# Performance work log

Hardware: AMD Instinct MI355X
Metric: run time of the kernel (lower is better)

Reference implementation:

```python
import jax, jax.numpy as jnp
import numpy as np

TEMPERATURE = 0.5
EPS = 1e-20


def setup_inputs() -> dict:
    key = jax.random.key(0)
    ks = jax.random.split(key, 7)
    N, T, S = 16, 64, 1024
    SRC, TGT, D = 512, 512, 64
    return {
        "input": jax.random.normal(ks[0], (N, T, TGT), jnp.float32),
        "memory_bank": jax.random.normal(ks[1], (N, S, SRC), jnp.float32),
        "W_q": jax.random.normal(ks[2], (TGT, D), jnp.float32) / np.sqrt(TGT),
        "W_ctx": jax.random.normal(ks[3], (SRC, D), jnp.float32) / np.sqrt(SRC),
        "v": jax.random.normal(ks[4], (D,), jnp.float32) / np.sqrt(D),
        "W_out": jax.random.normal(ks[5], (SRC + TGT, TGT), jnp.float32) / np.sqrt(SRC + TGT),
        "b_out": jax.random.normal(ks[6], (TGT,), jnp.float32) * 0.01,
    }


def reference(input, memory_bank, W_q, W_ctx, v, W_out, b_out):
    # MLP attention score: v^T tanh(W_q q + W_ctx h)
    wq = jnp.einsum("ntd,de->nte", input, W_q)            # [N,T,D]
    uh = jnp.einsum("nsd,de->nse", memory_bank, W_ctx)    # [N,S,D]
    wquh = jnp.tanh(wq[:, :, None, :] + uh[:, None, :, :])  # [N,T,S,D]
    scores = jnp.einsum("ntsd,d->nts", wquh, v)           # [N,T,S]

    log_alpha = jax.nn.log_softmax(scores, axis=-1)
    alpha = jnp.exp(log_alpha)                            # c_align_vectors

    # deterministic context + output
    context_c = jnp.einsum("nts,nsd->ntd", alpha, memory_bank)
    h_c = jnp.tanh(jnp.concatenate([input, context_c], axis=-1) @ W_out + b_out)

    # gumbel-softmax sample (K = n_samples = 1, forced by view_as in original)
    u = jax.random.uniform(jax.random.key(42), log_alpha.shape, jnp.float32)
    g = -jnp.log(-jnp.log(u + EPS) + EPS)                 # gumbel noise
    y_align = jax.nn.softmax((log_alpha + g) / TEMPERATURE, axis=-1)  # [N,T,S]

    context_y = jnp.einsum("nts,nsd->ntd", y_align, memory_bank)
    h_y = jnp.tanh(jnp.concatenate([input, context_y], axis=-1) @ W_out + b_out)

    return jnp.stack([h_c, h_y], axis=0)  # [2,N,T,tgt_dim]
```

## Files before the change

kernel.cpp:

```cpp
#include <hip/hip_runtime.h>
#include <hip/hip_bf16.h>
#include <stdint.h>

#define DEV __device__ __forceinline__

typedef __attribute__((ext_vector_type(8))) short short8;
typedef __attribute__((ext_vector_type(4))) float f32x4;

#define TWO_LOG2E 2.8853900817779268f

DEV unsigned short f2bf(float f) {
  uint32_t u = __float_as_uint(f);
  u += 0x7FFFu + ((u >> 16) & 1u);
  return (unsigned short)(u >> 16);
}

DEV uint2 pk4(float4 f) {
  union { __hip_bfloat162 h; unsigned u; } a, b;
  a.h = __float22bfloat162_rn(make_float2(f.x, f.y));
  b.h = __float22bfloat162_rn(make_float2(f.z, f.w));
  return make_uint2(a.u, b.u);
}

DEV short8 mk8(uint2 lo, uint2 hi) {
  union { short8 s; uint4 u; } t;
  t.u = make_uint4(lo.x, lo.y, hi.x, hi.y);
  return t.s;
}

DEV uint32_t rotl32(uint32_t x, int r) { return (x << r) | (x >> (32 - r)); }

DEV void threefry_0_42(uint32_t x0, uint32_t x1, uint32_t& o0, uint32_t& o1) {
  const uint32_t ks0 = 0u, ks1 = 42u, ks2 = 0x1BD11BDAu ^ 42u;
  x0 += ks0; x1 += ks1;
#define TFR(r) { x0 += x1; x1 = rotl32(x1, (r)); x1 ^= x0; }
  TFR(13) TFR(15) TFR(26) TFR(6)  x0 += ks1; x1 += ks2 + 1u;
  TFR(17) TFR(29) TFR(16) TFR(24) x0 += ks2; x1 += ks0 + 2u;
  TFR(13) TFR(15) TFR(26) TFR(6)  x0 += ks0; x1 += ks1 + 3u;
  TFR(17) TFR(29) TFR(16) TFR(24) x0 += ks1; x1 += ks2 + 4u;
  TFR(13) TFR(15) TFR(26) TFR(6)  x0 += ks2; x1 += ks0 + 5u;
#undef TFR
  o0 = x0; o1 = x1;
}

DEV float wredmax(float v) {
#pragma unroll
  for (int off = 32; off > 0; off >>= 1) v = fmaxf(v, __shfl_xor(v, off));
  return v;
}
DEV float wredsum(float v) {
#pragma unroll
  for (int off = 32; off > 0; off >>= 1) v += __shfl_xor(v, off);
  return v;
}

__global__ __launch_bounds__(256) void transpose_all(const float* __restrict__ Wctx,
                                                     const float* __restrict__ Wq,
                                                     const float* __restrict__ Wout,
                                                     unsigned short* __restrict__ WctxT,
                                                     unsigned short* __restrict__ WqT,
                                                     unsigned short* __restrict__ WoutT) {
  __shared__ float tile[64][65];
  const int b = blockIdx.x;
  const float* src; unsigned short* dst; int R, C, br, bc;
  if (b < 8)       { src = Wctx; dst = WctxT; R = 512;  C = 64;  br = b * 64;        bc = 0; }
  else if (b < 16) { src = Wq;   dst = WqT;   R = 512;  C = 64;  br = (b - 8) * 64;  bc = 0; }
  else { int i = b - 16; src = Wout; dst = WoutT; R = 1024; C = 512; br = (i & 15) * 64; bc = (i >> 4) * 64; }
  const int tid = threadIdx.x;
  const int lr = tid >> 4, lc4 = (tid & 15) * 4;
#pragma unroll
  for (int i = 0; i < 4; ++i) {
    float4 v = *(const float4*)(src + (long)(br + lr + i * 16) * C + bc + lc4);
    tile[lr + i * 16][lc4 + 0] = v.x;
    tile[lr + i * 16][lc4 + 1] = v.y;
    tile[lr + i * 16][lc4 + 2] = v.z;
    tile[lr + i * 16][lc4 + 3] = v.w;
  }
  __syncthreads();
#pragma unroll
  for (int i = 0; i < 4; ++i) {
    int crow = lr + i * 16;
    ushort4 o;
    o.x = f2bf(tile[lc4 + 0][crow]);
    o.y = f2bf(tile[lc4 + 1][crow]);
    o.z = f2bf(tile[lc4 + 2][crow]);
    o.w = f2bf(tile[lc4 + 3][crow]);
    *(ushort4*)(dst + (long)(bc + crow) * R + br + lc4) = o;
  }
}

__global__ __launch_bounds__(256) void gemm_uhwq(const float* __restrict__ mb,
                                                 const float* __restrict__ input,
                                                 const unsigned short* __restrict__ WctxT,
                                                 const unsigned short* __restrict__ WqT,
                                                 float* __restrict__ uhT,
                                                 float* __restrict__ wqo) {
  __shared__ unsigned short As[64][32];
  __shared__ unsigned short Bs[64][32];
  const int tid = threadIdx.x;
  const int bx = blockIdx.x;
  const float* A;  const unsigned short* BT;  int mbase;
  if (bx < 256) { A = mb;    BT = WctxT; mbase = bx * 64; }
  else          { A = input; BT = WqT;   mbase = (bx - 256) * 64; }
  const int srow = tid >> 2, kc = tid & 3;
  const int scol = ((kc ^ (srow & 3)) * 8);
  const int wave = tid >> 6, lane = tid & 63;
  const int wm = (wave >> 1) * 32, wn = (wave & 1) * 32;
  const int q = lane >> 4, r = lane & 15;
  const int c0 = ((q ^ (r & 3)) * 8);
  const float* ap = A + (long)(mbase + srow) * 512 + kc * 8;
  const unsigned short* bp = BT + (long)srow * 512 + kc * 8;
  f32x4 acc[2][2];
#pragma unroll
  for (int i = 0; i < 2; ++i)
#pragma unroll
    for (int j = 0; j < 2; ++j) acc[i][j] = (f32x4){0.f, 0.f, 0.f, 0.f};

  float4 fa0 = *(const float4*)(ap);
  float4 fa1 = *(const float4*)(ap + 4);
  uint4 fb = *(const uint4*)(bp);
  for (int k0 = 0; k0 < 512; k0 += 32) {
    uint2 p0 = pk4(fa0), p1 = pk4(fa1);
    *(uint4*)&As[srow][scol] = make_uint4(p0.x, p0.y, p1.x, p1.y);
    *(uint4*)&Bs[srow][scol] = fb;
    __syncthreads();
    if (k0 + 32 < 512) {
      fa0 = *(const float4*)(ap + k0 + 32);
      fa1 = *(const float4*)(ap + k0 + 36);
      fb = *(const uint4*)(bp + k0 + 32);
    }
    short8 a0 = *(const short8*)&As[wm + r][c0];
    short8 a1 = *(const short8*)&As[wm + 16 + r][c0];
    short8 b0 = *(const short8*)&Bs[wn + r][c0];
    short8 b1 = *(const short8*)&Bs[wn + 16 + r][c0];
    acc[0][0] = __builtin_amdgcn_mfma_f32_16x16x32_bf16(a0, b0, acc[0][0], 0, 0, 0);
    acc[0][1] = __builtin_amdgcn_mfma_f32_16x16x32_bf16(a0, b1, acc[0][1], 0, 0, 0);
    acc[1][0] = __builtin_amdgcn_mfma_f32_16x16x32_bf16(a1, b0, acc[1][0], 0, 0, 0);
    acc[1][1] = __builtin_amdgcn_mfma_f32_16x16x32_bf16(a1, b1, acc[1][1], 0, 0, 0);
    __syncthreads();
  }
#pragma unroll
  for (int i2 = 0; i2 < 2; ++i2)
#pragma unroll
    for (int j2 = 0; j2 < 2; ++j2) {
      int gcol = wn + j2 * 16 + r;
      int m = mbase + wm + i2 * 16 + q * 4;
      if (bx < 256) {
        int n = m >> 10, s0 = m & 1023;
        float4 o;
        o.x = acc[i2][j2][0] * TWO_LOG2E;
        o.y = acc[i2][j2][1] * TWO_LOG2E;
        o.z = acc[i2][j2][2] * TWO_LOG2E;
        o.w = acc[i2][j2][3] * TWO_LOG2E;
        *(float4*)(uhT + (long)n * 65536 + (long)gcol * 1024 + s0) = o;
      } else {
#pragma unroll
        for (int reg = 0; reg < 4; ++reg)
          wqo[(long)(m + reg) * 64 + gcol] = acc[i2][j2][reg] * TWO_LOG2E;
      }
    }
}

__global__ __launch_bounds__(256) void gemm_ctx_mfma(const float* __restrict__ alpha,
                                                     const float* __restrict__ yal,
                                                     const float* __restrict__ mb,
                                                     float* __restrict__ ctx) {
  __shared__ unsigned short As[64][32];
  const int tid = threadIdx.x;
  const int vt = blockIdx.x >> 4, n = blockIdx.x & 15;
  const int dbase = blockIdx.y * 32;
  const int srow = tid >> 2, kc = tid & 3;
  const int scol = ((kc ^ (srow & 3)) * 8);
  const int wave = tid >> 6, lane = tid & 63;
  const int wm = (wave >> 1) * 32, wn = (wave & 1) * 16;
  const int q = lane >> 4, r = lane & 15;
  const int c0 = ((q ^ (r & 3)) * 8);
  const float* Abase = (vt == 0 ? alpha : yal) + (long)n * 65536;
  const float* ap = Abase + (long)srow * 1024 + kc * 8;
  const float* bcol = mb + (long)n * 524288 + dbase + wn + r;
  f32x4 acc[2];
  acc[0] = (f32x4){0.f, 0.f, 0.f, 0.f};
  acc[1] = (f32x4){0.f, 0.f, 0.f, 0.f};

  float4 fa0 = *(const float4*)(ap);
  float4 fa1 = *(const float4*)(ap + 4);
  float bv[8];
#pragma unroll
  for (int j = 0; j < 8; ++j) bv[j] = bcol[(long)(q * 8 + j) * 512];

  for (int k0 = 0; k0 < 1024; k0 += 32) {
    uint2 p0 = pk4(fa0), p1 = pk4(fa1);
    *(uint4*)&As[srow][scol] = make_uint4(p0.x, p0.y, p1.x, p1.y);
    __syncthreads();
    float4 blo = make_float4(bv[0], bv[1], bv[2], bv[3]);
    float4 bhi = make_float4(bv[4], bv[5], bv[6], bv[7]);
    short8 b0 = mk8(pk4(blo), pk4(bhi));
    if (k0 + 32 < 1024) {
      fa0 = *(const float4*)(ap + k0 + 32);
      fa1 = *(const float4*)(ap + k0 + 36);
#pragma unroll
      for (int j = 0; j < 8; ++j) bv[j] = bcol[(long)(k0 + 32 + q * 8 + j) * 512];
    }
    short8 a0 = *(const short8*)&As[wm + r][c0];
    short8 a1 = *(const short8*)&As[wm + 16 + r][c0];
    acc[0] = __builtin_amdgcn_mfma_f32_16x16x32_bf16(a0, b0, acc[0], 0, 0, 0);
    acc[1] = __builtin_amdgcn_mfma_f32_16x16x32_bf16(a1, b0, acc[1], 0, 0, 0);
    __syncthreads();
  }
#pragma unroll
  for (int i2 = 0; i2 < 2; ++i2) {
    int gcol = dbase + wn + r;
#pragma unroll
    for (int reg = 0; reg < 4; ++reg) {
      long grow = (long)vt * 1024 + n * 64 + wm + i2 * 16 + q * 4 + reg;
      ctx[grow * 512 + gcol] = acc[i2][reg];
    }
  }
}

__global__ __launch_bounds__(256) void gemm_out_mfma(const float* __restrict__ input,
                                                     const float* __restrict__ ctx,
                                                     const unsigned short* __restrict__ WoutT,
                                                     const float* __restrict__ bout,
                                                     float* __restrict__ out) {
  __shared__ unsigned short As[64][32];
  __shared__ unsigned short Bs[32][32];
  const int tid = threadIdx.x;
  const int mbase = blockIdx.x * 64, nbase = blockIdx.y * 32;
  const int srow = tid >> 2, kc = tid & 3;
  const int scol = ((kc ^ (srow & 3)) * 8);
  const int wave = tid >> 6, lane = tid & 63;
  const int wm = (wave >> 1) * 32, wn = (wave & 1) * 16;
  const int q = lane >> 4, r = lane & 15;
  const int c0 = ((q ^ (r & 3)) * 8);
  const int vv = mbase >> 10, nt = (mbase + srow) & 1023;
  const float* ap_lo = input + (long)nt * 512 + kc * 8;
  const float* ap_hi = ctx + (long)(vv * 1024 + nt) * 512 + kc * 8 - 512;
  const int brow = (tid & 127) >> 2;
  const unsigned short* bp = WoutT + (long)(nbase + brow) * 1024 + kc * 8;
  f32x4 acc[2];
  acc[0] = (f32x4){0.f, 0.f, 0.f, 0.f};
  acc[1] = (f32x4){0.f, 0.f, 0.f, 0.f};

  float4 fa0 = *(const float4*)(ap_lo);
  float4 fa1 = *(const float4*)(ap_lo + 4);
  uint4 fb;
  if (tid < 128) fb = *(const uint4*)(bp);
  for (int k0 = 0; k0 < 1024; k0 += 32) {
    uint2 p0 = pk4(fa0), p1 = pk4(fa1);
    *(uint4*)&As[srow][scol] = make_uint4(p0.x, p0.y, p1.x, p1.y);
    if (tid < 128) *(uint4*)&Bs[brow][(kc ^ (brow & 3)) * 8] = fb;
    __syncthreads();
    int kn = k0 + 32;
    if (kn < 1024) {
      const float* apn = (kn < 512) ? ap_lo : ap_hi;
      fa0 = *(const float4*)(apn + kn);
      fa1 = *(const float4*)(apn + kn + 4);
      if (tid < 128) fb = *(const uint4*)(bp + kn);
    }
    short8 a0 = *(const short8*)&As[wm + r][c0];
    short8 a1 = *(const short8*)&As[wm + 16 + r][c0];
    short8 b0 = *(const short8*)&Bs[wn + r][c0];
    acc[0] = __builtin_amdgcn_mfma_f32_16x16x32_bf16(a0, b0, acc[0], 0, 0, 0);
    acc[1] = __builtin_amdgcn_mfma_f32_16x16x32_bf16(a1, b0, acc[1], 0, 0, 0);
    __syncthreads();
  }
#pragma unroll
  for (int i2 = 0; i2 < 2; ++i2) {
    int gcol = nbase + wn + r;
    float bb = bout[gcol];
#pragma unroll
    for (int reg = 0; reg < 4; ++reg) {
      int grow = mbase + wm + i2 * 16 + q * 4 + reg;
      float z = acc[i2][reg] + bb;
      float rc = __builtin_amdgcn_rcpf(1.f + __builtin_amdgcn_exp2f(z * TWO_LOG2E));
      out[(long)grow * 512 + gcol] = fmaf(-2.f, rc, 1.f);
    }
  }
}

__global__ __launch_bounds__(256) void scores_kernel(const float* __restrict__ uhT,
                                                     const float* __restrict__ wq2,
                                                     const float* __restrict__ v,
                                                     float* __restrict__ alpha_g,
                                                     float* __restrict__ y_g) {
  const int tid = threadIdx.x;
  const int nt = blockIdx.x;
  const int n = nt >> 6;
  __shared__ float wvs[64];
  __shared__ float vvs[64];
  __shared__ float red[4];
  if (tid < 64) {
    wvs[tid] = wq2[nt * 64 + tid];
    vvs[tid] = v[tid];
  }
  __syncthreads();

  float sumv = 0.f;
#pragma unroll
  for (int d = 0; d < 64; d += 4) {
    float4 vv = *(const float4*)&vvs[d];
    sumv += vv.x + vv.y + vv.z + vv.w;
  }

  const float* un = uhT + (long)n * 65536 + tid * 4;
  float4 racc = make_float4(0.f, 0.f, 0.f, 0.f);
  for (int db = 0; db < 64; db += 8) {
    float4 ub[8];
#pragma unroll
    for (int j = 0; j < 8; ++j) ub[j] = *(const float4*)(un + (long)(db + j) * 1024);
#pragma unroll
    for (int j = 0; j < 8; ++j) {
      float w = wvs[db + j], vvj = vvs[db + j];
      racc.x = fmaf(vvj, __builtin_amdgcn_rcpf(1.f + __builtin_amdgcn_exp2f(ub[j].x + w)), racc.x);
      racc.y = fmaf(vvj, __builtin_amdgcn_rcpf(1.f + __builtin_amdgcn_exp2f(ub[j].y + w)), racc.y);
      racc.z = fmaf(vvj, __builtin_amdgcn_rcpf(1.f + __builtin_amdgcn_exp2f(ub[j].z + w)), racc.z);
      racc.w = fmaf(vvj, __builtin_amdgcn_rcpf(1.f + __builtin_amdgcn_exp2f(ub[j].w + w)), racc.w);
    }
  }
  float lsc[4];
  lsc[0] = fmaf(-2.f, racc.x, sumv);
  lsc[1] = fmaf(-2.f, racc.y, sumv);
  lsc[2] = fmaf(-2.f, racc.z, sumv);
  lsc[3] = fmaf(-2.f, racc.w, sumv);

  const int wv = tid >> 6, ln = tid & 63;
  float m = fmaxf(fmaxf(lsc[0], lsc[1]), fmaxf(lsc[2], lsc[3]));
  m = wredmax(m);
  if (ln == 0) red[wv] = m;
  __syncthreads();
  m = fmaxf(fmaxf(red[0], red[1]), fmaxf(red[2], red[3]));
  __syncthreads();
  float ss = 0.f;
#pragma unroll
  for (int i = 0; i < 4; ++i) ss += __expf(lsc[i] - m);
  ss = wredsum(ss);
  if (ln == 0) red[wv] = ss;
  __syncthreads();
  ss = red[0] + red[1] + red[2] + red[3];
  const float logl = __logf(ss);
  __syncthreads();

  const uint32_t jbase = (uint32_t)nt * 1024u + (uint32_t)tid * 4u;
  float ys[4];
  float4 av;
#pragma unroll
  for (int i = 0; i < 4; ++i) {
    float la = lsc[i] - m - logl;
    ((float*)&av)[i] = __expf(la);
    uint32_t o0, o1;
    threefry_0_42(0u, jbase + i, o0, o1);
    uint32_t bits = o0 ^ o1;
    float u = __uint_as_float((bits >> 9) | 0x3f800000u) - 1.0f;
    float g = -__logf(-__logf(u + 1e-20f) + 1e-20f);
    ys[i] = (la + g) * 2.0f;
  }
  *(float4*)(alpha_g + (long)nt * 1024 + tid * 4) = av;

  float m2 = fmaxf(fmaxf(ys[0], ys[1]), fmaxf(ys[2], ys[3]));
  m2 = wredmax(m2);
  if (ln == 0) red[wv] = m2;
  __syncthreads();
  m2 = fmaxf(fmaxf(red[0], red[1]), fmaxf(red[2], red[3]));
  __syncthreads();
  float s2 = 0.f;
  float4 ye;
#pragma unroll
  for (int i = 0; i < 4; ++i) { ((float*)&ye)[i] = __expf(ys[i] - m2); s2 += ((float*)&ye)[i]; }
  s2 = wredsum(s2);
  if (ln == 0) red[wv] = s2;
  __syncthreads();
  s2 = red[0] + red[1] + red[2] + red[3];
  const float rinv = __fdividef(1.f, s2);
  ye.x *= rinv; ye.y *= rinv; ye.z *= rinv; ye.w *= rinv;
  *(float4*)(y_g + (long)nt * 1024 + tid * 4) = ye;
}

extern "C" void kernel_launch(void* const* d_in, const int* in_sizes, int n_in,
                              void* d_out, int out_size, void* d_ws, size_t ws_size,
                              hipStream_t stream) {
  const float* input = (const float*)d_in[0];
  const float* mb    = (const float*)d_in[1];
  const float* W_q   = (const float*)d_in[2];
  const float* W_ctx = (const float*)d_in[3];
  const float* v     = (const float*)d_in[4];
  const float* W_out = (const float*)d_in[5];
  const float* b_out = (const float*)d_in[6];
  float* out = (float*)d_out;
  float* ws = (float*)d_ws;

  float* uhT   = ws;
  float* wq    = ws + 1048576;
  float* yal   = ws + 1114112;
  unsigned short* WctxT = (unsigned short*)(ws + 2162688);
  unsigned short* WqT   = (unsigned short*)(ws + 2179072);
  unsigned short* WoutT = (unsigned short*)(ws + 2195456);
  float* alpha = out;
  float* ctx   = uhT;

  transpose_all<<<144, 256, 0, stream>>>(W_ctx, W_q, W_out, WctxT, WqT, WoutT);
  gemm_uhwq<<<272, 256, 0, stream>>>(mb, input, WctxT, WqT, uhT, wq);
  scores_kernel<<<1024, 256, 0, stream>>>(uhT, wq, v, alpha, yal);
  gemm_ctx_mfma<<<dim3(32, 16), 256, 0, stream>>>(alpha, yal, mb, ctx);
  gemm_out_mfma<<<dim3(32, 16), 256, 0, stream>>>(input, ctx, WoutT, b_out, out);
}
```

Before: 153.6 us.

## Fuse uh GEMM with MLP score computation and split out softmax/gumbel kernel

The memory-bank projection GEMM now computes the tanh-based scores directly from its tile held in shared memory, so the uh intermediate is never written to or read back from global memory. The wq projection moves into the prep kernel, which reads W_q directly and drops the W_q transpose. The softmax and Gumbel sampling move into their own kernel that reads the stored scores. The fused kernel does the full S×T×D transcendental work in only 256 blocks with a heavy shared-memory footprint (~42KB), so parallelism and occupancy drop compared with the old 1024-block scores kernel.

```diff
diff --git a/kernel.cpp b/kernel.cpp
--- a/kernel.cpp
+++ b/kernel.cpp
@@ -54,62 +54,119 @@
   return v;
 }
 
-__global__ __launch_bounds__(256) void transpose_all(const float* __restrict__ Wctx,
-                                                     const float* __restrict__ Wq,
-                                                     const float* __restrict__ Wout,
-                                                     unsigned short* __restrict__ WctxT,
-                                                     unsigned short* __restrict__ WqT,
-                                                     unsigned short* __restrict__ WoutT) {
+__global__ __launch_bounds__(256) void prep_kernel(const float* __restrict__ Wctx,
+                                                   const float* __restrict__ Wq,
+                                                   const float* __restrict__ Wout,
+                                                   const float* __restrict__ input,
+                                                   unsigned short* __restrict__ WctxT,
+                                                   unsigned short* __restrict__ WoutT,
+                                                   float* __restrict__ wq2) {
+  const int b = blockIdx.x;
+  const int tid = threadIdx.x;
   __shared__ float tile[64][65];
-  const int b = blockIdx.x;
-  const float* src; unsigned short* dst; int R, C, br, bc;
-  if (b < 8)       { src = Wctx; dst = WctxT; R = 512;  C = 64;  br = b * 64;        bc = 0; }
-  else if (b < 16) { src = Wq;   dst = WqT;   R = 512;  C = 64;  br = (b - 8) * 64;  bc = 0; }
-  else { int i = b - 16; src = Wout; dst = WoutT; R = 1024; C = 512; br = (i & 15) * 64; bc = (i >> 4) * 64; }
-  const int tid = threadIdx.x;
-  const int lr = tid >> 4, lc4 = (tid & 15) * 4;
-#pragma unroll
-  for (int i = 0; i < 4; ++i) {
-    float4 v = *(const float4*)(src + (long)(br + lr + i * 16) * C + bc + lc4);
-    tile[lr + i * 16][lc4 + 0] = v.x;
-    tile[lr + i * 16][lc4 + 1] = v.y;
-    tile[lr + i * 16][lc4 + 2] = v.z;
-    tile[lr + i * 16][lc4 + 3] = v.w;
-  }
-  __syncthreads();
-#pragma unroll
-  for (int i = 0; i < 4; ++i) {
-    int crow = lr + i * 16;
-    ushort4 o;
-    o.x = f2bf(tile[lc4 + 0][crow]);
-    o.y = f2bf(tile[lc4 + 1][crow]);
-    o.z = f2bf(tile[lc4 + 2][crow]);
-    o.w = f2bf(tile[lc4 + 3][crow]);
-    *(ushort4*)(dst + (long)(bc + crow) * R + br + lc4) = o;
-  }
-}
-
-__global__ __launch_bounds__(256) void gemm_uhwq(const float* __restrict__ mb,
-                                                 const float* __restrict__ input,
-                                                 const unsigned short* __restrict__ WctxT,
-                                                 const unsigned short* __restrict__ WqT,
-                                                 float* __restrict__ uhT,
-                                                 float* __restrict__ wqo) {
   __shared__ unsigned short As[64][32];
-  __shared__ unsigned short Bs[64][32];
-  const int tid = threadIdx.x;
-  const int bx = blockIdx.x;
-  const float* A;  const unsigned short* BT;  int mbase;
-  if (bx < 256) { A = mb;    BT = WctxT; mbase = bx * 64; }
-  else          { A = input; BT = WqT;   mbase = (bx - 256) * 64; }
+  if (b < 136) {
+    const float* src; unsigned short* dst; int R, C, br, bc;
+    if (b < 128) { src = Wout; dst = WoutT; R = 1024; C = 512; br = (b & 15) * 64; bc = (b >> 4) * 64; }
+    else         { src = Wctx; dst = WctxT; R = 512;  C = 64;  br = (b - 128) * 64; bc = 0; }
+    const int lr = tid >> 4, lc4 = (tid & 15) * 4;
+#pragma unroll
+    for (int i = 0; i < 4; ++i) {
+      float4 v = *(const float4*)(src + (long)(br + lr + i * 16) * C + bc + lc4);
+      tile[lr + i * 16][lc4 + 0] = v.x;
+      tile[lr + i * 16][lc4 + 1] = v.y;
+      tile[lr + i * 16][lc4 + 2] = v.z;
+      tile[lr + i * 16][lc4 + 3] = v.w;
+    }
+    __syncthreads();
+#pragma unroll
+    for (int i = 0; i < 4; ++i) {
+      int crow = lr + i * 16;
+      ushort4 o;
+      o.x = f2bf(tile[lc4 + 0][crow]);
+      o.y = f2bf(tile[lc4 + 1][crow]);
+      o.z = f2bf(tile[lc4 + 2][crow]);
+      o.w = f2bf(tile[lc4 + 3][crow]);
+      *(ushort4*)(dst + (long)(bc + crow) * R + br + lc4) = o;
+    }
+    return;
+  }
+  const int mbase = (b - 136) * 64;
   const int srow = tid >> 2, kc = tid & 3;
   const int scol = ((kc ^ (srow & 3)) * 8);
   const int wave = tid >> 6, lane = tid & 63;
   const int wm = (wave >> 1) * 32, wn = (wave & 1) * 32;
   const int q = lane >> 4, r = lane & 15;
   const int c0 = ((q ^ (r & 3)) * 8);
-  const float* ap = A + (long)(mbase + srow) * 512 + kc * 8;
-  const unsigned short* bp = BT + (long)srow * 512 + kc * 8;
+  const float* ap = input + (long)(mbase + srow) * 512 + kc * 8;
+  f32x4 acc[2][2];
+#pragma unroll
+  for (int i = 0; i < 2; ++i)
+#pragma unroll
+    for (int j = 0; j < 2; ++j) acc[i][j] = (f32x4){0.f, 0.f, 0.f, 0.f};
+  for (int k0 = 0; k0 < 512; k0 += 32) {
+    float4 fa0 = *(const float4*)(ap + k0);
+    float4 fa1 = *(const float4*)(ap + k0 + 4);
+    uint2 p0 = pk4(fa0), p1 = pk4(fa1);
+    *(uint4*)&As[srow][scol] = make_uint4(p0.x, p0.y, p1.x, p1.y);
+    __syncthreads();
+    short8 bfrag[2];
+#pragma unroll
+    for (int j2 = 0; j2 < 2; ++j2) {
+      float bv[8];
+#pragma unroll
+      for (int j = 0; j < 8; ++j)
+        bv[j] = Wq[(long)(k0 + q * 8 + j) * 64 + wn + j2 * 16 + r];
+      bfrag[j2] = mk8(pk4(make_float4(bv[0], bv[1], bv[2], bv[3])),
+                      pk4(make_float4(bv[4], bv[5], bv[6], bv[7])));
+    }
+    short8 a0 = *(const short8*)&As[wm + r][c0];
+    short8 a1 = *(const short8*)&As[wm + 16 + r][c0];
+    acc[0][0] = __builtin_amdgcn_mfma_f32_16x16x32_bf16(a0, bfrag[0], acc[0][0], 0, 0, 0);
+    acc[0][1] = __builtin_amdgcn_mfma_f32_16x16x32_bf16(a0, bfrag[1], acc[0][1], 0, 0, 0);
+    acc[1][0] = __builtin_amdgcn_mfma_f32_16x16x32_bf16(a1, bfrag[0], acc[1][0], 0, 0, 0);
+    acc[1][1] = __builtin_amdgcn_mfma_f32_16x16x32_bf16(a1, bfrag[1], acc[1][1], 0, 0, 0);
+    __syncthreads();
+  }
+#pragma unroll
+  for (int i2 = 0; i2 < 2; ++i2)
+#pragma unroll
+    for (int j2 = 0; j2 < 2; ++j2) {
+      int gcol = wn + j2 * 16 + r;
+#pragma unroll
+      for (int reg = 0; reg < 4; ++reg)
+        wq2[(long)(mbase + wm + i2 * 16 + q * 4 + reg) * 64 + gcol] =
+            acc[i2][j2][reg] * TWO_LOG2E;
+    }
+}
+
+__global__ __launch_bounds__(256) void gemm_uh_scores(const float* __restrict__ mb,
+                                                      const unsigned short* __restrict__ WctxT,
+                                                      const float* __restrict__ wq2,
+                                                      const float* __restrict__ v,
+                                                      float* __restrict__ sc) {
+  __shared__ unsigned short As[64][32];
+  __shared__ unsigned short Bs[64][32];
+  __shared__ float uhs[64][65];
+  __shared__ float wqs[4096];
+  __shared__ float vs[64];
+  const int tid = threadIdx.x;
+  const int m0 = blockIdx.x * 64;
+  const int n = m0 >> 10, s0 = m0 & 1023;
+  const int srow = tid >> 2, kc = tid & 3;
+  const int scol = ((kc ^ (srow & 3)) * 8);
+  const int wave = tid >> 6, lane = tid & 63;
+  const int wm = (wave >> 1) * 32, wn = (wave & 1) * 32;
+  const int q = lane >> 4, r = lane & 15;
+  const int c0 = ((q ^ (r & 3)) * 8);
+  const float* ap = mb + (long)(m0 + srow) * 512 + kc * 8;
+  const unsigned short* bp = WctxT + (long)srow * 512 + kc * 8;
+
+#pragma unroll
+  for (int i = 0; i < 4; ++i)
+    *(float4*)&wqs[i * 1024 + tid * 4] = *(const float4*)(wq2 + (long)n * 4096 + i * 1024 + tid * 4);
+  if (tid < 64) vs[tid] = v[tid];
+
   f32x4 acc[2][2];
 #pragma unroll
   for (int i = 0; i < 2; ++i)
@@ -142,23 +199,102 @@
 #pragma unroll
   for (int i2 = 0; i2 < 2; ++i2)
 #pragma unroll
-    for (int j2 = 0; j2 < 2; ++j2) {
-      int gcol = wn + j2 * 16 + r;
-      int m = mbase + wm + i2 * 16 + q * 4;
-      if (bx < 256) {
-        int n = m >> 10, s0 = m & 1023;
-        float4 o;
-        o.x = acc[i2][j2][0] * TWO_LOG2E;
-        o.y = acc[i2][j2][1] * TWO_LOG2E;
-        o.z = acc[i2][j2][2] * TWO_LOG2E;
-        o.w = acc[i2][j2][3] * TWO_LOG2E;
-        *(float4*)(uhT + (long)n * 65536 + (long)gcol * 1024 + s0) = o;
-      } else {
-#pragma unroll
-        for (int reg = 0; reg < 4; ++reg)
-          wqo[(long)(m + reg) * 64 + gcol] = acc[i2][j2][reg] * TWO_LOG2E;
-      }
-    }
+    for (int j2 = 0; j2 < 2; ++j2)
+#pragma unroll
+      for (int reg = 0; reg < 4; ++reg)
+        uhs[wm + i2 * 16 + q * 4 + reg][wn + j2 * 16 + r] = acc[i2][j2][reg] * TWO_LOG2E;
+  __syncthreads();
+
+  const int s = tid & 63;
+  const int tbase = (tid >> 6) * 16;
+  float sumv = 0.f;
+#pragma unroll
+  for (int c = 0; c < 64; c += 4) {
+    float4 vv = *(const float4*)&vs[c];
+    sumv += vv.x + vv.y + vv.z + vv.w;
+  }
+  float* scp = sc + (long)(n * 64 + tbase) * 1024 + s0 + s;
+#pragma unroll
+  for (int tg = 0; tg < 16; tg += 4) {
+    const float* w0 = &wqs[(tbase + tg + 0) * 64];
+    const float* w1 = &wqs[(tbase + tg + 1) * 64];
+    const float* w2 = &wqs[(tbase + tg + 2) * 64];
+    const float* w3 = &wqs[(tbase + tg + 3) * 64];
+    float a0 = 0.f, a1 = 0.f, a2 = 0.f, a3 = 0.f;
+    for (int c = 0; c < 64; ++c) {
+      float u = uhs[s][c];
+      float vvc = vs[c];
+      a0 = fmaf(vvc, __builtin_amdgcn_rcpf(1.f + __builtin_amdgcn_exp2f(u + w0[c])), a0);
+      a1 = fmaf(vvc, __builtin_amdgcn_rcpf(1.f + __builtin_amdgcn_exp2f(u + w1[c])), a1);
+      a2 = fmaf(vvc, __builtin_amdgcn_rcpf(1.f + __builtin_amdgcn_exp2f(u + w2[c])), a2);
+      a3 = fmaf(vvc, __builtin_amdgcn_rcpf(1.f + __builtin_amdgcn_exp2f(u + w3[c])), a3);
+    }
+    scp[(long)(tg + 0) * 1024] = fmaf(-2.f, a0, sumv);
+    scp[(long)(tg + 1) * 1024] = fmaf(-2.f, a1, sumv);
+    scp[(long)(tg + 2) * 1024] = fmaf(-2.f, a2, sumv);
+    scp[(long)(tg + 3) * 1024] = fmaf(-2.f, a3, sumv);
+  }
+}
+
+__global__ __launch_bounds__(256) void softmax_gumbel(const float* __restrict__ sc,
+                                                      float* __restrict__ alpha_g,
+                                                      float* __restrict__ y_g) {
+  const int tid = threadIdx.x;
+  const int nt = blockIdx.x;
+  __shared__ float red[4];
+  float4 l4 = *(const float4*)(sc + (long)nt * 1024 + tid * 4);
+  float lsc[4] = {l4.x, l4.y, l4.z, l4.w};
+
+  const int wv = tid >> 6, ln = tid & 63;
+  float m = fmaxf(fmaxf(lsc[0], lsc[1]), fmaxf(lsc[2], lsc[3]));
+  m = wredmax(m);
+  if (ln == 0) red[wv] = m;
+  __syncthreads();
+  m = fmaxf(fmaxf(red[0], red[1]), fmaxf(red[2], red[3]));
+  __syncthreads();
+  float ss = 0.f;
+#pragma unroll
+  for (int i = 0; i < 4; ++i) ss += __expf(lsc[i] - m);
+  ss = wredsum(ss);
+  if (ln == 0) red[wv] = ss;
+  __syncthreads();
+  ss = red[0] + red[1] + red[2] + red[3];
+  const float logl = __logf(ss);
+  __syncthreads();
+
+  const uint32_t jbase = (uint32_t)nt * 1024u + (uint32_t)tid * 4u;
+  float ys[4];
+  float4 av;
+#pragma unroll
+  for (int i = 0; i < 4; ++i) {
+    float la = lsc[i] - m - logl;
+    ((float*)&av)[i] = __expf(la);
+    uint32_t o0, o1;
+    threefry_0_42(0u, jbase + i, o0, o1);
+    uint32_t bits = o0 ^ o1;
+    float u = __uint_as_float((bits >> 9) | 0x3f800000u) - 1.0f;
+    float g = -__logf(-__logf(u + 1e-20f) + 1e-20f);
+    ys[i] = (la + g) * 2.0f;
+  }
+  *(float4*)(alpha_g + (long)nt * 1024 + tid * 4) = av;
+
+  float m2 = fmaxf(fmaxf(ys[0], ys[1]), fmaxf(ys[2], ys[3]));
+  m2 = wredmax(m2);
+  if (ln == 0) red[wv] = m2;
+  __syncthreads();
+  m2 = fmaxf(fmaxf(red[0], red[1]), fmaxf(red[2], red[3]));
+  __syncthreads();
+  float s2 = 0.f;
+  float4 ye;
+#pragma unroll
+  for (int i = 0; i < 4; ++i) { ((float*)&ye)[i] = __expf(ys[i] - m2); s2 += ((float*)&ye)[i]; }
+  s2 = wredsum(s2);
+  if (ln == 0) red[wv] = s2;
+  __syncthreads();
+  s2 = red[0] + red[1] + red[2] + red[3];
+  const float rinv = __fdividef(1.f, s2);
+  ye.x *= rinv; ye.y *= rinv; ye.z *= rinv; ye.w *= rinv;
+  *(float4*)(y_g + (long)nt * 1024 + tid * 4) = ye;
 }
 
 __global__ __launch_bounds__(256) void gemm_ctx_mfma(const float* __restrict__ alpha,
@@ -279,103 +415,6 @@
   }
 }
 
-__global__ __launch_bounds__(256) void scores_kernel(const float* __restrict__ uhT,
-                                                     const float* __restrict__ wq2,
-                                                     const float* __restrict__ v,
-                                                     float* __restrict__ alpha_g,
-                                                     float* __restrict__ y_g) {
-  const int tid = threadIdx.x;
-  const int nt = blockIdx.x;
-  const int n = nt >> 6;
-  __shared__ float wvs[64];
-  __shared__ float vvs[64];
-  __shared__ float red[4];
-  if (tid < 64) {
-    wvs[tid] = wq2[nt * 64 + tid];
-    vvs[tid] = v[tid];
-  }
-  __syncthreads();
-
-  float sumv = 0.f;
-#pragma unroll
-  for (int d = 0; d < 64; d += 4) {
-    float4 vv = *(const float4*)&vvs[d];
-    sumv += vv.x + vv.y + vv.z + vv.w;
-  }
-
-  const float* un = uhT + (long)n * 65536 + tid * 4;
-  float4 racc = make_float4(0.f, 0.f, 0.f, 0.f);
-  for (int db = 0; db < 64; db += 8) {
-    float4 ub[8];
-#pragma unroll
-    for (int j = 0; j < 8; ++j) ub[j] = *(const float4*)(un + (long)(db + j) * 1024);
-#pragma unroll
-    for (int j = 0; j < 8; ++j) {
-      float w = wvs[db + j], vvj = vvs[db + j];
-      racc.x = fmaf(vvj, __builtin_amdgcn_rcpf(1.f + __builtin_amdgcn_exp2f(ub[j].x + w)), racc.x);
-      racc.y = fmaf(vvj, __builtin_amdgcn_rcpf(1.f + __builtin_amdgcn_exp2f(ub[j].y + w)), racc.y);
-      racc.z = fmaf(vvj, __builtin_amdgcn_rcpf(1.f + __builtin_amdgcn_exp2f(ub[j].z + w)), racc.z);
-      racc.w = fmaf(vvj, __builtin_amdgcn_rcpf(1.f + __builtin_amdgcn_exp2f(ub[j].w + w)), racc.w);
-    }
-  }
-  float lsc[4];
-  lsc[0] = fmaf(-2.f, racc.x, sumv);
-  lsc[1] = fmaf(-2.f, racc.y, sumv);
-  lsc[2] = fmaf(-2.f, racc.z, sumv);
-  lsc[3] = fmaf(-2.f, racc.w, sumv);
-
-  const int wv = tid >> 6, ln = tid & 63;
-  float m = fmaxf(fmaxf(lsc[0], lsc[1]), fmaxf(lsc[2], lsc[3]));
-  m = wredmax(m);
-  if (ln == 0) red[wv] = m;
-  __syncthreads();
-  m = fmaxf(fmaxf(red[0], red[1]), fmaxf(red[2], red[3]));
-  __syncthreads();
-  float ss = 0.f;
-#pragma unroll
-  for (int i = 0; i < 4; ++i) ss += __expf(lsc[i] - m);
-  ss = wredsum(ss);
-  if (ln == 0) red[wv] = ss;
-  __syncthreads();
-  ss = red[0] + red[1] + red[2] + red[3];
-  const float logl = __logf(ss);
-  __syncthreads();
-
-  const uint32_t jbase = (uint32_t)nt * 1024u + (uint32_t)tid * 4u;
-  float ys[4];
-  float4 av;
-#pragma unroll
-  for (int i = 0; i < 4; ++i) {
-    float la = lsc[i] - m - logl;
-    ((float*)&av)[i] = __expf(la);
-    uint32_t o0, o1;
-    threefry_0_42(0u, jbase + i, o0, o1);
-    uint32_t bits = o0 ^ o1;
-    float u = __uint_as_float((bits >> 9) | 0x3f800000u) - 1.0f;
-    float g = -__logf(-__logf(u + 1e-20f) + 1e-20f);
-    ys[i] = (la + g) * 2.0f;
-  }
-  *(float4*)(alpha_g + (long)nt * 1024 + tid * 4) = av;
-
-  float m2 = fmaxf(fmaxf(ys[0], ys[1]), fmaxf(ys[2], ys[3]));
-  m2 = wredmax(m2);
-  if (ln == 0) red[wv] = m2;
-  __syncthreads();
-  m2 = fmaxf(fmaxf(red[0], red[1]), fmaxf(red[2], red[3]));
-  __syncthreads();
-  float s2 = 0.f;
-  float4 ye;
-#pragma unroll
-  for (int i = 0; i < 4; ++i) { ((float*)&ye)[i] = __expf(ys[i] - m2); s2 += ((float*)&ye)[i]; }
-  s2 = wredsum(s2);
-  if (ln == 0) red[wv] = s2;
-  __syncthreads();
-  s2 = red[0] + red[1] + red[2] + red[3];
-  const float rinv = __fdividef(1.f, s2);
-  ye.x *= rinv; ye.y *= rinv; ye.z *= rinv; ye.w *= rinv;
-  *(float4*)(y_g + (long)nt * 1024 + tid * 4) = ye;
-}
-
 extern "C" void kernel_launch(void* const* d_in, const int* in_sizes, int n_in,
                               void* d_out, int out_size, void* d_ws, size_t ws_size,
                               hipStream_t stream) {
@@ -389,18 +428,17 @@
   float* out = (float*)d_out;
   float* ws = (float*)d_ws;
 
-  float* uhT   = ws;
-  float* wq    = ws + 1048576;
+  float* sc    = ws;
+  float* wq2   = ws + 1048576;
   float* yal   = ws + 1114112;
   unsigned short* WctxT = (unsigned short*)(ws + 2162688);
-  unsigned short* WqT   = (unsigned short*)(ws + 2179072);
-  unsigned short* WoutT = (unsigned short*)(ws + 2195456);
+  unsigned short* WoutT = (unsigned short*)(ws + 2179072);
   float* alpha = out;
-  float* ctx   = uhT;
-
-  transpose_all<<<144, 256, 0, stream>>>(W_ctx, W_q, W_out, WctxT, WqT, WoutT);
-  gemm_uhwq<<<272, 256, 0, stream>>>(mb, input, WctxT, WqT, uhT, wq);
-  scores_kernel<<<1024, 256, 0, stream>>>(uhT, wq, v, alpha, yal);
+  float* ctx   = sc;
+
+  prep_kernel<<<152, 256, 0, stream>>>(W_ctx, W_q, W_out, input, WctxT, WoutT, wq2);
+  gemm_uh_scores<<<256, 256, 0, stream>>>(mb, WctxT, wq2, v, sc);
+  softmax_gumbel<<<1024, 256, 0, stream>>>(sc, alpha, yal);
   gemm_ctx_mfma<<<dim3(32, 16), 256, 0, stream>>>(alpha, yal, mb, ctx);
   gemm_out_mfma<<<dim3(32, 16), 256, 0, stream>>>(input, ctx, WoutT, b_out, out);
 }
```

Result: slower. 174.3 us (+13.5%).
